# Kernel tuning notes

Hardware: AMD Instinct MI355X
Metric: run time of the kernel (lower is better)

## Reference

```python
import jax, jax.numpy as jnp
import numpy as np

# Planck radiance in wavenumber form: B(nu, T) = c1*nu^3 / (exp(c2*nu/T) - 1)
# nu in cm^-1, T in Kelvin, B in W / (m^2 sr cm^-1)
C1 = 1.191042e-8
C2 = 1.4387752
N_TEMPS = 20


def planck_radiance(nu, T):
    return C1 * nu ** 3 / jnp.expm1(C2 * nu / T)


def setup_inputs() -> dict:
    key = jax.random.key(0)
    k1, k2, k3 = jax.random.split(key, 3)
    N, C = 1048576, 54  # 1024x1024 pixels, 54 spectral channels
    wg = jnp.linspace(720.0, 1250.0, C, dtype=jnp.float32)
    v = (wg - wg.min()) / (wg.max() - wg.min())
    pi = 3.14159
    library = jnp.stack([
        jnp.full((C,), 0.98),                      # skin
        0.9 + 0.05 * jnp.sin(2 * pi * v),          # fabric_cotton
        0.15 + 0.1 * v,                            # metal_aluminum
        0.95 - 0.03 * v,                           # vegetation
        0.92 + 0.02 * jnp.sin(4 * pi * v),         # concrete
        0.85 + 0.1 * v,                            # glass
    ]).astype(jnp.float32)
    # realistic LWIR radiance magnitudes (~0.02-0.12 W/m^2/sr/cm^-1)
    s_sky = 0.05 * jax.random.uniform(k1, (C,), dtype=jnp.float32)
    s_ground = 0.08 + 0.02 * jax.random.uniform(k2, (C,), dtype=jnp.float32)
    s_obs = 0.02 + 0.1 * jax.random.uniform(k3, (N, C), dtype=jnp.float32)
    return {"s_obs": s_obs, "s_sky": s_sky, "s_ground": s_ground,
            "library": library, "wavenumber_grid": wg}


def reference(s_obs, s_sky, s_ground, library, wavenumber_grid):
    N, C = s_obs.shape
    M = library.shape[0]
    t_cand = jnp.linspace(250.0, 350.0, N_TEMPS, dtype=s_obs.dtype)
    # All candidate model spectra are pixel-independent (V fixed at 0.5):
    x_amb = 0.5 * s_sky + 0.5 * s_ground                           # [C]
    B = planck_radiance(wavenumber_grid[None, :], t_cand[:, None])  # [T, C]
    s_model = library[:, None, :] * B[None, :, :] \
        + (1.0 - library[:, None, :]) * x_amb                       # [M, T, C]
    cand = s_model.reshape(M * N_TEMPS, C)  # row-major: idx = m*T + t, matches loop order
    # ||s_obs - cand||^2 expanded: memory-bound [N, M*T] loss matrix
    losses = (jnp.sum(s_obs ** 2, axis=-1, keepdims=True)
              - 2.0 * s_obs @ cand.T
              + jnp.sum(cand ** 2, axis=-1))                        # [N, M*T]
    best = jnp.argmin(losses, axis=-1)                              # first-min, matches strict '<'
    best_loss = jnp.take_along_axis(losses, best[:, None], axis=1)[:, 0]
    m_idx = best // N_TEMPS
    t_idx = best % N_TEMPS
    best_t = t_cand[t_idx]                                          # [N]
    best_e = library[m_idx]                                         # [N, C]
    best_v = jnp.full((N,), 0.5, dtype=s_obs.dtype)
    s_recon = best_e * planck_radiance(wavenumber_grid[None, :], best_t[:, None]) \
        + (1.0 - best_e) * x_amb                                    # [N, C]
    texture = best_e.mean(axis=-1)
    beta = jnp.zeros((N, 1), dtype=s_obs.dtype)
    objective = best_loss.mean()
    return (best_t, best_e, best_v, beta, texture, s_recon, objective)
```

## Files before the change

kernel.cpp:

```cpp
#include <hip/hip_runtime.h>
#include <math.h>

#define C_CH 54
#define CP   56
#define NT   20
#define NM   6
#define NK   120
#define PIX  3
#define BLK  256
#define PPB  (BLK * PIX)

__global__ __launch_bounds__(BLK, 2) void hadar_main(
    const float* __restrict__ s_obs,
    const float* __restrict__ s_sky, const float* __restrict__ s_ground,
    const float* __restrict__ library, const float* __restrict__ wg,
    float* __restrict__ out, float* __restrict__ partials, int N)
{
    __shared__ __align__(16) float cand[NK * CP];
    __shared__ float candsq[NK];
    __shared__ float tc[NT];
    __shared__ float xamb[C_CH];
    __shared__ float libl[NM * C_CH];
    __shared__ float libmean[NM];

    const int tid = threadIdx.x;
    const long long base = (long long)blockIdx.x * PPB + tid;

    float row[PIX][CP];
    bool  valid[PIX];
    #pragma unroll
    for (int p = 0; p < PIX; ++p) {
        const long long np = base + (long long)p * BLK;
        valid[p] = (np < N);
        row[p][54] = 0.0f; row[p][55] = 0.0f;
        if (valid[p]) {
            const float2* rp = (const float2*)(s_obs + np * C_CH);
            #pragma unroll
            for (int i = 0; i < C_CH / 2; ++i) {
                float2 v = rp[i];
                row[p][2 * i] = v.x; row[p][2 * i + 1] = v.y;
            }
        } else {
            #pragma unroll
            for (int c = 0; c < C_CH; ++c) row[p][c] = 0.0f;
        }
    }

    if (tid < NT) tc[tid] = 250.0f + (float)tid * (100.0f / 19.0f);
    if (tid < C_CH) xamb[tid] = 0.5f * s_sky[tid] + 0.5f * s_ground[tid];
    for (int i = tid; i < NM * C_CH; i += BLK) libl[i] = library[i];
    __syncthreads();

    const float c1 = 1.191042e-8f, c2 = 1.4387752f;
    for (int idx = tid; idx < NK * CP; idx += BLK) {
        const int k = idx / CP, c = idx - k * CP;
        float v = 0.0f;
        if (c < C_CH) {
            const int m = k / NT, t = k - m * NT;
            const float nu = wg[c];
            const float B = c1 * nu * nu * nu / expm1f(c2 * nu / tc[t]);
            const float e = libl[m * C_CH + c];
            v = e * B + (1.0f - e) * xamb[c];
        }
        cand[idx] = v;
    }
    __syncthreads();

    if (tid < NK) {
        float s = 0.0f;
        for (int c = 0; c < C_CH; ++c) { float v = cand[tid * CP + c]; s += v * v; }
        candsq[tid] = s;
    }
    if (tid < NM) {
        float s = 0.0f;
        for (int c = 0; c < C_CH; ++c) s += libl[tid * C_CH + c];
        libmean[tid] = s / (float)C_CH;
    }
    __syncthreads();

    float ssq[PIX];
    #pragma unroll
    for (int p = 0; p < PIX; ++p) {
        float s = 0.0f;
        #pragma unroll
        for (int c = 0; c < C_CH; ++c) s += row[p][c] * row[p][c];
        ssq[p] = s;
    }

    float best_loss[PIX];
    int   bestk[PIX];
    #pragma unroll
    for (int p = 0; p < PIX; ++p) { best_loss[p] = 3.4e38f; bestk[p] = 0; }

    #pragma unroll 2
    for (int k = 0; k < NK; ++k) {
        const float* ck = cand + k * CP;
        float a[PIX][4];
        #pragma unroll
        for (int p = 0; p < PIX; ++p)
            { a[p][0] = 0.f; a[p][1] = 0.f; a[p][2] = 0.f; a[p][3] = 0.f; }
        #pragma unroll
        for (int c = 0; c < CP; c += 4) {
            const float4 q = *(const float4*)(ck + c);
            #pragma unroll
            for (int p = 0; p < PIX; ++p) {
                a[p][0] += row[p][c + 0] * q.x;
                a[p][1] += row[p][c + 1] * q.y;
                a[p][2] += row[p][c + 2] * q.z;
                a[p][3] += row[p][c + 3] * q.w;
            }
        }
        #pragma unroll
        for (int p = 0; p < PIX; ++p) {
            const float dot = (a[p][0] + a[p][1]) + (a[p][2] + a[p][3]);
            const float loss = (ssq[p] - 2.0f * dot) + candsq[k];
            if (loss < best_loss[p]) { best_loss[p] = loss; bestk[p] = k; }
        }
    }

    const size_t NN = (size_t)N;
    const size_t NC = (size_t)C_CH * NN;
    float lsum = 0.0f;
    #pragma unroll
    for (int p = 0; p < PIX; ++p) {
        const long long np = base + (long long)p * BLK;
        if (!valid[p]) continue;
        lsum += best_loss[p];
        const int m = bestk[p] / NT, t = bestk[p] - m * NT;

        out[np] = tc[t];
        out[NN + NC + np] = 0.5f;
        out[2 * NN + NC + np] = 0.0f;
        out[3 * NN + NC + np] = libmean[m];

        float2* bep = (float2*)(out + NN + (size_t)np * C_CH);
        const float2* lp = (const float2*)(libl + m * C_CH);
        #pragma unroll
        for (int i = 0; i < C_CH / 2; ++i) bep[i] = lp[i];

        float2* srp = (float2*)(out + 4 * NN + NC + (size_t)np * C_CH);
        const float2* cp2 = (const float2*)(cand + bestk[p] * CP);
        #pragma unroll
        for (int i = 0; i < C_CH / 2; ++i) srp[i] = cp2[i];
    }

    __shared__ float red[BLK];
    red[tid] = lsum;
    __syncthreads();
    #pragma unroll
    for (int s = BLK / 2; s > 0; s >>= 1) {
        if (tid < s) red[tid] += red[tid + s];
        __syncthreads();
    }
    if (tid == 0) partials[blockIdx.x] = red[0];
}

__global__ __launch_bounds__(256) void hadar_reduce(
    const float* __restrict__ partials, int nb, float* __restrict__ obj_out, float invN)
{
    __shared__ float red[256];
    float s = 0.0f;
    for (int i = threadIdx.x; i < nb; i += 256) s += partials[i];
    red[threadIdx.x] = s;
    __syncthreads();
    #pragma unroll
    for (int st = 128; st > 0; st >>= 1) {
        if (threadIdx.x < st) red[threadIdx.x] += red[threadIdx.x + st];
        __syncthreads();
    }
    if (threadIdx.x == 0) *obj_out = red[0] * invN;
}

extern "C" void kernel_launch(void* const* d_in, const int* in_sizes, int n_in,
                              void* d_out, int out_size, void* d_ws, size_t ws_size,
                              hipStream_t stream)
{
    const float* s_obs    = (const float*)d_in[0];
    const float* s_sky    = (const float*)d_in[1];
    const float* s_ground = (const float*)d_in[2];
    const float* library  = (const float*)d_in[3];
    const float* wg       = (const float*)d_in[4];
    float* out = (float*)d_out;

    const int N  = in_sizes[0] / C_CH;
    const int nb = (N + PPB - 1) / PPB;

    float* partials = (float*)d_ws;

    hadar_main<<<nb, BLK, 0, stream>>>(s_obs, s_sky, s_ground, library, wg,
                                       out, partials, N);

    const size_t NN = (size_t)N;
    float* obj_out = out + 4 * NN + 2 * (size_t)C_CH * NN;
    hadar_reduce<<<1, 256, 0, stream>>>(partials, nb, obj_out, 1.0f / (float)N);
}
```

Before: 914.7 us.

## Precompute candidates in prep kernel and stream them via scalar loads

```diff
diff --git a/kernel.cpp b/kernel.cpp
--- a/kernel.cpp
+++ b/kernel.cpp
@@ -2,64 +2,44 @@
 #include <math.h>
 
 #define C_CH 54
-#define CP   56
+#define CP   64
 #define NT   20
 #define NM   6
 #define NK   120
-#define PIX  3
+#define PIX  2
 #define BLK  256
 #define PPB  (BLK * PIX)
 
-__global__ __launch_bounds__(BLK, 2) void hadar_main(
-    const float* __restrict__ s_obs,
+typedef float sf16 __attribute__((ext_vector_type(16)));
+typedef float sf8  __attribute__((ext_vector_type(8)));
+
+__global__ __launch_bounds__(256) void hadar_prep(
     const float* __restrict__ s_sky, const float* __restrict__ s_ground,
     const float* __restrict__ library, const float* __restrict__ wg,
-    float* __restrict__ out, float* __restrict__ partials, int N)
-{
-    __shared__ __align__(16) float cand[NK * CP];
-    __shared__ float candsq[NK];
+    float* __restrict__ cand)
+{
+    __shared__ float xamb[C_CH];
     __shared__ float tc[NT];
-    __shared__ float xamb[C_CH];
-    __shared__ float libl[NM * C_CH];
-    __shared__ float libmean[NM];
-
+    __shared__ float lm[NM];
     const int tid = threadIdx.x;
-    const long long base = (long long)blockIdx.x * PPB + tid;
-
-    float row[PIX][CP];
-    bool  valid[PIX];
-    #pragma unroll
-    for (int p = 0; p < PIX; ++p) {
-        const long long np = base + (long long)p * BLK;
-        valid[p] = (np < N);
-        row[p][54] = 0.0f; row[p][55] = 0.0f;
-        if (valid[p]) {
-            const float2* rp = (const float2*)(s_obs + np * C_CH);
-            #pragma unroll
-            for (int i = 0; i < C_CH / 2; ++i) {
-                float2 v = rp[i];
-                row[p][2 * i] = v.x; row[p][2 * i + 1] = v.y;
-            }
-        } else {
-            #pragma unroll
-            for (int c = 0; c < C_CH; ++c) row[p][c] = 0.0f;
-        }
-    }
-
     if (tid < NT) tc[tid] = 250.0f + (float)tid * (100.0f / 19.0f);
     if (tid < C_CH) xamb[tid] = 0.5f * s_sky[tid] + 0.5f * s_ground[tid];
-    for (int i = tid; i < NM * C_CH; i += BLK) libl[i] = library[i];
+    if (tid < NM) {
+        float s = 0.0f;
+        for (int c = 0; c < C_CH; ++c) s += library[tid * C_CH + c];
+        lm[tid] = s / (float)C_CH;
+    }
     __syncthreads();
 
     const float c1 = 1.191042e-8f, c2 = 1.4387752f;
-    for (int idx = tid; idx < NK * CP; idx += BLK) {
-        const int k = idx / CP, c = idx - k * CP;
+    for (int idx = tid; idx < NK * CP; idx += 256) {
+        const int k = idx >> 6, c = idx & 63;
         float v = 0.0f;
         if (c < C_CH) {
             const int m = k / NT, t = k - m * NT;
             const float nu = wg[c];
             const float B = c1 * nu * nu * nu / expm1f(c2 * nu / tc[t]);
-            const float e = libl[m * C_CH + c];
+            const float e = library[m * C_CH + c];
             v = e * B + (1.0f - e) * xamb[c];
         }
         cand[idx] = v;
@@ -69,77 +49,113 @@
     if (tid < NK) {
         float s = 0.0f;
         for (int c = 0; c < C_CH; ++c) { float v = cand[tid * CP + c]; s += v * v; }
-        candsq[tid] = s;
-    }
-    if (tid < NM) {
-        float s = 0.0f;
-        for (int c = 0; c < C_CH; ++c) s += libl[tid * C_CH + c];
-        libmean[tid] = s / (float)C_CH;
-    }
-    __syncthreads();
-
-    float ssq[PIX];
-    #pragma unroll
-    for (int p = 0; p < PIX; ++p) {
-        float s = 0.0f;
-        #pragma unroll
-        for (int c = 0; c < C_CH; ++c) s += row[p][c] * row[p][c];
-        ssq[p] = s;
-    }
-
-    float best_loss[PIX];
-    int   bestk[PIX];
-    #pragma unroll
-    for (int p = 0; p < PIX; ++p) { best_loss[p] = 3.4e38f; bestk[p] = 0; }
-
-    #pragma unroll 2
-    for (int k = 0; k < NK; ++k) {
-        const float* ck = cand + k * CP;
-        float a[PIX][4];
-        #pragma unroll
-        for (int p = 0; p < PIX; ++p)
-            { a[p][0] = 0.f; a[p][1] = 0.f; a[p][2] = 0.f; a[p][3] = 0.f; }
-        #pragma unroll
-        for (int c = 0; c < CP; c += 4) {
-            const float4 q = *(const float4*)(ck + c);
-            #pragma unroll
-            for (int p = 0; p < PIX; ++p) {
-                a[p][0] += row[p][c + 0] * q.x;
-                a[p][1] += row[p][c + 1] * q.y;
-                a[p][2] += row[p][c + 2] * q.z;
-                a[p][3] += row[p][c + 3] * q.w;
-            }
-        }
-        #pragma unroll
-        for (int p = 0; p < PIX; ++p) {
-            const float dot = (a[p][0] + a[p][1]) + (a[p][2] + a[p][3]);
-            const float loss = (ssq[p] - 2.0f * dot) + candsq[k];
-            if (loss < best_loss[p]) { best_loss[p] = loss; bestk[p] = k; }
-        }
+        const int m = tid / NT, t = tid - m * NT;
+        cand[tid * CP + 54] = s;
+        cand[tid * CP + 55] = tc[t];
+        cand[tid * CP + 56] = lm[m];
+    }
+}
+
+#define CE(c) ((c) < 16 ? q0[(c)] : (c) < 32 ? q1[(c)-16] : (c) < 48 ? q2[(c)-32] : q3[(c)-48])
+
+__global__ __launch_bounds__(BLK, 3) void hadar_main(
+    const float* __restrict__ s_obs,
+    const float* __restrict__ library,
+    const float* __restrict__ cand,
+    float* __restrict__ out, float* __restrict__ partials, int N)
+{
+    const int tid = threadIdx.x;
+    const long long n0 = (long long)blockIdx.x * PPB + tid;
+    const long long n1 = n0 + BLK;
+    const bool v0 = (n0 < N), v1 = (n1 < N);
+
+    float row0[C_CH], row1[C_CH];
+    if (v0) {
+        const float2* rp = (const float2*)(s_obs + n0 * C_CH);
+        #pragma unroll
+        for (int i = 0; i < C_CH / 2; ++i) {
+            float2 w = rp[i];
+            row0[2 * i] = w.x; row0[2 * i + 1] = w.y;
+        }
+    } else {
+        #pragma unroll
+        for (int c = 0; c < C_CH; ++c) row0[c] = 0.0f;
+    }
+    if (v1) {
+        const float2* rp = (const float2*)(s_obs + n1 * C_CH);
+        #pragma unroll
+        for (int i = 0; i < C_CH / 2; ++i) {
+            float2 w = rp[i];
+            row1[2 * i] = w.x; row1[2 * i + 1] = w.y;
+        }
+    } else {
+        #pragma unroll
+        for (int c = 0; c < C_CH; ++c) row1[c] = 0.0f;
+    }
+
+    float ssq0 = 0.0f, ssq1 = 0.0f;
+    #pragma unroll
+    for (int c = 0; c < C_CH; ++c) ssq0 += row0[c] * row0[c];
+    #pragma unroll
+    for (int c = 0; c < C_CH; ++c) ssq1 += row1[c] * row1[c];
+
+    float bl0 = 3.4e38f, bl1 = 3.4e38f;
+    int bk0 = 0, bk1 = 0;
+
+    const float* pk = cand;
+    for (int k = 0; k < NK; ++k, pk += CP) {
+        sf16 q0, q1, q2;
+        sf8  q3;
+        asm volatile("s_load_dwordx16 %0, %1, 0x0"  : "=s"(q0) : "s"(pk));
+        asm volatile("s_load_dwordx16 %0, %1, 0x40" : "=s"(q1) : "s"(pk));
+        asm volatile("s_load_dwordx16 %0, %1, 0x80" : "=s"(q2) : "s"(pk));
+        asm volatile("s_load_dwordx8  %0, %1, 0xc0" : "=s"(q3) : "s"(pk));
+        asm volatile("s_waitcnt lgkmcnt(0)" : "+s"(q0), "+s"(q1), "+s"(q2), "+s"(q3));
+
+        float a0[4] = {0.f, 0.f, 0.f, 0.f};
+        float a1[4] = {0.f, 0.f, 0.f, 0.f};
+        #pragma unroll
+        for (int c = 0; c < C_CH; ++c) {
+            const float cv = CE(c);
+            a0[c & 3] += row0[c] * cv;
+            a1[c & 3] += row1[c] * cv;
+        }
+        const float sq = q3[6];
+        const float d0 = (a0[0] + a0[1]) + (a0[2] + a0[3]);
+        const float d1 = (a1[0] + a1[1]) + (a1[2] + a1[3]);
+        const float l0 = (ssq0 - 2.0f * d0) + sq;
+        const float l1 = (ssq1 - 2.0f * d1) + sq;
+        if (l0 < bl0) { bl0 = l0; bk0 = k; }
+        if (l1 < bl1) { bl1 = l1; bk1 = k; }
     }
 
     const size_t NN = (size_t)N;
     const size_t NC = (size_t)C_CH * NN;
     float lsum = 0.0f;
+
     #pragma unroll
     for (int p = 0; p < PIX; ++p) {
-        const long long np = base + (long long)p * BLK;
-        if (!valid[p]) continue;
-        lsum += best_loss[p];
-        const int m = bestk[p] / NT, t = bestk[p] - m * NT;
-
-        out[np] = tc[t];
+        const long long np = (p == 0) ? n0 : n1;
+        const bool vp = (p == 0) ? v0 : v1;
+        const int bk = (p == 0) ? bk0 : bk1;
+        const float bl = (p == 0) ? bl0 : bl1;
+        if (!vp) continue;
+        lsum += bl;
+        const int m = bk / NT;
+        const float* crow = cand + (size_t)bk * CP;
+
+        out[np] = crow[55];
         out[NN + NC + np] = 0.5f;
         out[2 * NN + NC + np] = 0.0f;
-        out[3 * NN + NC + np] = libmean[m];
+        out[3 * NN + NC + np] = crow[56];
 
         float2* bep = (float2*)(out + NN + (size_t)np * C_CH);
-        const float2* lp = (const float2*)(libl + m * C_CH);
+        const float2* lp = (const float2*)(library + m * C_CH);
         #pragma unroll
         for (int i = 0; i < C_CH / 2; ++i) bep[i] = lp[i];
 
         float2* srp = (float2*)(out + 4 * NN + NC + (size_t)np * C_CH);
-        const float2* cp2 = (const float2*)(cand + bestk[p] * CP);
+        const float2* cp2 = (const float2*)crow;
         #pragma unroll
         for (int i = 0; i < C_CH / 2; ++i) srp[i] = cp2[i];
     }
@@ -185,10 +201,12 @@
     const int N  = in_sizes[0] / C_CH;
     const int nb = (N + PPB - 1) / PPB;
 
-    float* partials = (float*)d_ws;
-
-    hadar_main<<<nb, BLK, 0, stream>>>(s_obs, s_sky, s_ground, library, wg,
-                                       out, partials, N);
+    float* ws       = (float*)d_ws;
+    float* cand     = ws;
+    float* partials = ws + 8192;
+
+    hadar_prep<<<1, 256, 0, stream>>>(s_sky, s_ground, library, wg, cand);
+    hadar_main<<<nb, BLK, 0, stream>>>(s_obs, library, cand, out, partials, N);
 
     const size_t NN = (size_t)N;
     float* obj_out = out + 4 * NN + 2 * (size_t)C_CH * NN;
```

Measured after the change: 835.9 us. -8.6%, faster.
